# Kernel tuning notes

Measured on AMD Instinct MI355X. Metric: run time of the kernel, lower is better.

Reference implementation:

```python
import jax, jax.numpy as jnp
import numpy as np

NUM_USER = 100000
NUM_ITEM = 50000
N_NODES = NUM_USER + NUM_ITEM
DIM_E = 64
N_EDGES = 2_000_000  # user-item interactions; symmetric adj nnz = 2*N_EDGES
N_LAYERS = 3
DROP_RATE = 0.5
BATCH = 16384


def setup_inputs() -> dict:
    key = jax.random.key(0)
    k_u, k_i, k_ue, k_ie, k_m, k_bu, k_bi = jax.random.split(key, 7)
    # bipartite interaction edges -> symmetric adjacency (COO)
    u = jax.random.randint(k_u, (N_EDGES,), 0, NUM_USER, dtype=jnp.int32)
    it = jax.random.randint(k_i, (N_EDGES,), 0, NUM_ITEM, dtype=jnp.int32) + NUM_USER
    adj_row = jnp.concatenate([u, it])          # [4M]
    adj_col = jnp.concatenate([it, u])          # [4M]
    # symmetric normalization D^-1/2 A D^-1/2
    deg = jnp.zeros((N_NODES,), jnp.float32).at[adj_row].add(1.0) + 1e-7
    dinv = deg ** -0.5
    adj_val = dinv[adj_row] * dinv[adj_col]     # [4M]
    # xavier-uniform-ish embeddings
    ue_scale = (6.0 / (NUM_USER + DIM_E)) ** 0.5
    ie_scale = (6.0 / (NUM_ITEM + DIM_E)) ** 0.5
    user_emb = jax.random.uniform(k_ue, (NUM_USER, DIM_E), jnp.float32, -ue_scale, ue_scale)
    item_emb = jax.random.uniform(k_ie, (NUM_ITEM, DIM_E), jnp.float32, -ie_scale, ie_scale)
    # fixed sparse-dropout keep mask (rate=0.5)
    drop_mask = jax.random.uniform(k_m, (2 * N_EDGES,)) < (1.0 - DROP_RATE)
    users = jax.random.randint(k_bu, (BATCH,), 0, NUM_USER, dtype=jnp.int64)
    items = jax.random.randint(k_bi, (BATCH,), 0, NUM_ITEM, dtype=jnp.int64)
    return {"user_emb": user_emb, "item_emb": item_emb, "adj_val": adj_val,
            "adj_row": adj_row, "adj_col": adj_col, "drop_mask": drop_mask,
            "users": users, "items": items}


def reference(user_emb, item_emb, adj_val, adj_row, adj_col, drop_mask, users, items):
    # sparse dropout: drop entries, rescale kept ones by 1/(1-rate)
    val = jnp.where(drop_mask, adj_val * (1.0 / (1.0 - DROP_RATE)), 0.0)
    ego = jnp.concatenate([user_emb, item_emb], axis=0)   # [N, D]
    acc = ego
    for _ in range(N_LAYERS):
        # SpMM: out[r] += val * ego[c]
        ego = jax.ops.segment_sum(val[:, None] * ego[adj_col], adj_row,
                                  num_segments=N_NODES)
        acc = acc + ego
    all_emb = acc / (N_LAYERS + 1)                        # mean over stacked layers
    user_embeddings = all_emb[users]
    item_embeddings = all_emb[NUM_USER + items]
    return (user_embeddings, item_embeddings)
```

## Files before the change

### kernel.cpp

```cpp
#include <hip/hip_runtime.h>
#include <hip/hip_bf16.h>


#define NUSER 100000
#define NITEM 50000
#define NNODE 150000
#define DIM   64
#define NNZ   4000000
#define BATCH 16384

#define BSH2  9
#define BRWS  512
#define NBK   293
#define SCAP  2048
#define BCAP  16384
#define CHUNK 2048

typedef __hip_bfloat16 bf16;
typedef unsigned short ushort;
typedef unsigned long long u64;
typedef float f4 __attribute__((ext_vector_type(4)));
typedef ushort us4 __attribute__((ext_vector_type(4)));
typedef ushort us8 __attribute__((ext_vector_type(8)));

__device__ __forceinline__ float loadF(const void* p, long i, int isbf16) {
    return isbf16 ? __bfloat162float(((const bf16*)p)[i]) : ((const float*)p)[i];
}

__device__ __forceinline__ bool keepE(const void* mask, int e, int isbyte) {
    return isbyte ? (((const unsigned char*)mask)[e] != 0)
                  : (((const int*)mask)[e] != 0);
}

__device__ __forceinline__ ushort f2bf(float x) {
    unsigned u = __float_as_uint(x);
    return (ushort)((u + 0x7FFFu + ((u >> 16) & 1u)) >> 16);
}
__device__ __forceinline__ float bf2f(ushort u) {
    return __uint_as_float((unsigned)u << 16);
}

__device__ __forceinline__ unsigned encodeV(float v) {
    unsigned fb = __float_as_uint(v);
    unsigned e8 = (fb >> 23) & 0xFFu;
    unsigned m7 = (fb >> 16) & 0x7Fu;
    return ((e8 - 95u) << 7) | m7;
}
__device__ __forceinline__ float decodeV(unsigned code) {
    unsigned vb = code >> 18;
    return __uint_as_float((((vb >> 7) + 95u) << 23) | ((vb & 0x7Fu) << 16));
}

__global__ __launch_bounds__(256) void detect_fmt(const unsigned int* __restrict__ mask,
                                                  const unsigned int* __restrict__ users,
                                                  const unsigned int* __restrict__ adjv,
                                                  int* __restrict__ flags,
                                                  int* __restrict__ bcur) {
    __shared__ int s[3];
    if (threadIdx.x < 3) s[threadIdx.x] = 0;
    for (int b = threadIdx.x; b < 8 * NBK; b += 256) bcur[b] = 0;
    __syncthreads();
    int c0 = 0, c1 = 0, c2 = 0;
    for (int i = threadIdx.x; i < 4096; i += 256) {
        c0 += (mask[i] > 1u) ? 1 : 0;
        if (i & 1) c1 += (users[i] == 0u) ? 1 : 0;
        unsigned lo = adjv[i] & 0xFFFFu;
        unsigned ex = (lo >> 7) & 0xFFu;
        c2 += ((lo >> 15) == 0u && ex >= 0x60u && ex <= 0x7Fu) ? 1 : 0;
    }
    atomicAdd(&s[0], c0); atomicAdd(&s[1], c1); atomicAdd(&s[2], c2);
    __syncthreads();
    if (threadIdx.x == 0) {
        flags[0] = (s[0] > 16) ? 1 : 0;
        flags[1] = (s[1] > 1024) ? 1 : 0;
        flags[2] = (s[2] > 3000) ? 1 : 0;
    }
}

__global__ __launch_bounds__(256) void pass1_partition(const void* __restrict__ mask,
                                                       const int* __restrict__ rows,
                                                       const int* __restrict__ cols,
                                                       const void* __restrict__ adjv,
                                                       const int* __restrict__ flags,
                                                       int* __restrict__ bcur,
                                                       u64* __restrict__ part) {
    __shared__ int cnt[NBK];
    __shared__ int cur[NBK];
    const int isbyte = flags[0];
    const int isbf = flags[2];
    const int base_e = blockIdx.x * CHUNK;
    const int sh = blockIdx.x & 7;
    u64 rec[8];
    int bkt[8];
    unsigned kept = 0;

    for (int b = threadIdx.x; b < NBK; b += 256) cnt[b] = 0;
    __syncthreads();

    #pragma unroll
    for (int k = 0; k < 8; ++k) {
        int e = base_e + k * 256 + threadIdx.x;
        if (e < NNZ && keepE(mask, e, isbyte)) {
            int r = rows[e];
            float v = 2.0f * loadF(adjv, e, isbf);
            rec[k] = (u64)(unsigned)(r & (BRWS - 1))
                   | ((u64)(unsigned)cols[e] << 9)
                   | ((u64)encodeV(v) << 27);
            bkt[k] = r >> BSH2;
            kept |= 1u << k;
            atomicAdd(&cnt[bkt[k]], 1);
        }
    }
    __syncthreads();

    for (int b = threadIdx.x; b < NBK; b += 256)
        cur[b] = cnt[b] ? atomicAdd(&bcur[sh * NBK + b], cnt[b]) : 0;
    __syncthreads();

    #pragma unroll
    for (int k = 0; k < 8; ++k) {
        if (kept & (1u << k)) {
            int pos = atomicAdd(&cur[bkt[k]], 1);
            if (pos < SCAP)
                part[(size_t)bkt[k] * BCAP + sh * SCAP + pos] = rec[k];
        }
    }
}

__global__ __launch_bounds__(512) void bucket_scan(const int* __restrict__ bcur,
                                                   int* __restrict__ gbase,
                                                   int* __restrict__ rowptr) {
    __shared__ int s[512];
    int tid = threadIdx.x;
    int v = 0;
    if (tid < NBK) {
        #pragma unroll
        for (int sh = 0; sh < 8; ++sh) {
            int c = bcur[sh * NBK + tid];
            v += (c > SCAP) ? SCAP : c;
        }
    }
    s[tid] = v;
    __syncthreads();
    for (int off = 1; off < 512; off <<= 1) {
        int t = (tid >= off) ? s[tid - off] : 0;
        __syncthreads();
        s[tid] += t;
        __syncthreads();
    }
    if (tid < NBK) gbase[tid] = s[tid] - v;
    if (tid == 0) rowptr[0] = 0;
}

__global__ __launch_bounds__(512) void pass2_csr(const u64* __restrict__ part,
                                                 const int* __restrict__ bcur,
                                                 const int* __restrict__ gbase,
                                                 unsigned* __restrict__ edges,
                                                 int* __restrict__ rowptr) {
    __shared__ int cnt[BRWS];
    __shared__ int ex[BRWS];
    __shared__ int wsum[512];
    __shared__ int ns[8];
    int b = blockIdx.x;
    int tid = threadIdx.x;
    if (tid < 8) {
        int c = bcur[tid * NBK + b];
        ns[tid] = (c > SCAP) ? SCAP : c;
    }
    const u64* bp = part + (size_t)b * BCAP;
    int gb = gbase[b];

    cnt[tid] = 0;
    __syncthreads();
    #pragma unroll
    for (int sh = 0; sh < 8; ++sh) {
        int n = ns[sh];
        const u64* rp = bp + sh * SCAP;
        for (int j = tid; j < n; j += 512)
            atomicAdd(&cnt[(int)(rp[j] & (BRWS - 1))], 1);
    }
    __syncthreads();

    int c = cnt[tid];
    wsum[tid] = c;
    __syncthreads();
    for (int off = 1; off < 512; off <<= 1) {
        int t = (tid >= off) ? wsum[tid - off] : 0;
        __syncthreads();
        wsum[tid] += t;
        __syncthreads();
    }
    int incl = wsum[tid];
    ex[tid] = incl - c;
    int gr = (b << BSH2) + tid;
    if (gr < NNODE) rowptr[gr + 1] = gb + incl;
    __syncthreads();

    #pragma unroll
    for (int sh = 0; sh < 8; ++sh) {
        int n = ns[sh];
        const u64* rp = bp + sh * SCAP;
        for (int j = tid; j < n; j += 512) {
            u64 rec = rp[j];
            int r = (int)(rec & (BRWS - 1));
            int pos = atomicAdd(&ex[r], 1);
            unsigned col = (unsigned)((rec >> 9) & 0x3FFFFu);
            unsigned code = (unsigned)((rec >> 27) & 0x1FFFu);
            edges[gb + pos] = col | (code << 18);
        }
    }
}

__global__ __launch_bounds__(256) void concat_cast(const void* __restrict__ ue,
                                                   const void* __restrict__ ie,
                                                   const int* __restrict__ flags,
                                                   ushort* __restrict__ A) {
    long q = (long)blockIdx.x * 256 + threadIdx.x;
    const long NU4 = (long)NUSER * DIM / 4;
    const long NT4 = (long)NNODE * DIM / 4;
    if (q >= NT4) return;
    us4 o;
    if (!flags[2]) {
        const f4* s = (q < NU4) ? (const f4*)ue : (const f4*)ie;
        f4 v = s[(q < NU4) ? q : q - NU4];
        o[0] = f2bf(v.x); o[1] = f2bf(v.y); o[2] = f2bf(v.z); o[3] = f2bf(v.w);
    } else {
        const us4* s = (q < NU4) ? (const us4*)ue : (const us4*)ie;
        o = s[(q < NU4) ? q : q - NU4];
    }
    ((us4*)A)[q] = o;
}

__global__ __launch_bounds__(256) void spmm_csr(const ushort* __restrict__ src,
                                                const int* __restrict__ rowptr,
                                                const unsigned* __restrict__ edges,
                                                ushort* __restrict__ dst) {
    int r = blockIdx.x * 32 + (threadIdx.x >> 3);
    if (r >= NNODE) return;
    int t = threadIdx.x & 7;
    int j0 = rowptr[r], j1 = rowptr[r + 1];
    float acc[8] = {0, 0, 0, 0, 0, 0, 0, 0};
    int j = j0;
    for (; j + 4 <= j1; j += 4) {
        unsigned e0 = edges[j];
        unsigned e1 = edges[j + 1];
        unsigned e2 = edges[j + 2];
        unsigned e3 = edges[j + 3];
        us8 s0 = ((const us8*)(src + (size_t)(e0 & 0x3FFFFu) * DIM))[t];
        us8 s1 = ((const us8*)(src + (size_t)(e1 & 0x3FFFFu) * DIM))[t];
        us8 s2 = ((const us8*)(src + (size_t)(e2 & 0x3FFFFu) * DIM))[t];
        us8 s3 = ((const us8*)(src + (size_t)(e3 & 0x3FFFFu) * DIM))[t];
        float v0 = decodeV(e0), v1 = decodeV(e1);
        float v2 = decodeV(e2), v3 = decodeV(e3);
        #pragma unroll
        for (int d = 0; d < 8; ++d) {
            acc[d] += v0 * bf2f(s0[d]);
            acc[d] += v1 * bf2f(s1[d]);
            acc[d] += v2 * bf2f(s2[d]);
            acc[d] += v3 * bf2f(s3[d]);
        }
    }
    for (; j < j1; ++j) {
        unsigned e0 = edges[j];
        float v0 = decodeV(e0);
        us8 s0 = ((const us8*)(src + (size_t)(e0 & 0x3FFFFu) * DIM))[t];
        #pragma unroll
        for (int d = 0; d < 8; ++d) acc[d] += v0 * bf2f(s0[d]);
    }
    us8 o;
    #pragma unroll
    for (int d = 0; d < 8; ++d) o[d] = f2bf(acc[d]);
    __builtin_nontemporal_store(o, (us8*)(dst + (size_t)r * DIM) + t);
}

__device__ __forceinline__ long nodeOf(int b, const int* users, const int* items, int sh) {
    if (b < BATCH) return (long)users[(size_t)b << sh];
    return (long)NUSER + (long)items[(size_t)(b - BATCH) << sh];
}

__global__ __launch_bounds__(256) void gather_first(const ushort* __restrict__ table,
                                                    const int* __restrict__ users,
                                                    const int* __restrict__ items,
                                                    const int* __restrict__ flags,
                                                    float* __restrict__ acc) {
    int t = blockIdx.x * 256 + threadIdx.x;
    if (t >= 2 * BATCH * DIM / 4) return;
    long node = nodeOf(t >> 4, users, items, flags[1]);
    us4 u = ((const us4*)(table + node * DIM))[t & 15];
    f4 a = {bf2f(u[0]), bf2f(u[1]), bf2f(u[2]), bf2f(u[3])};
    ((f4*)acc)[t] = a;
}

__global__ __launch_bounds__(256) void gather_add(const ushort* __restrict__ table,
                                                  const int* __restrict__ users,
                                                  const int* __restrict__ items,
                                                  const int* __restrict__ flags,
                                                  float* __restrict__ acc) {
    int t = blockIdx.x * 256 + threadIdx.x;
    if (t >= 2 * BATCH * DIM / 4) return;
    long node = nodeOf(t >> 4, users, items, flags[1]);
    us4 u = ((const us4*)(table + node * DIM))[t & 15];
    f4 a = ((f4*)acc)[t];
    a.x += bf2f(u[0]); a.y += bf2f(u[1]); a.z += bf2f(u[2]); a.w += bf2f(u[3]);
    ((f4*)acc)[t] = a;
}

__global__ __launch_bounds__(256) void gather_final(const ushort* __restrict__ table,
                                                    const int* __restrict__ users,
                                                    const int* __restrict__ items,
                                                    const int* __restrict__ flags,
                                                    const float* __restrict__ acc,
                                                    float* __restrict__ out) {
    int t = blockIdx.x * 256 + threadIdx.x;
    if (t >= 2 * BATCH * DIM / 4) return;
    long node = nodeOf(t >> 4, users, items, flags[1]);
    us4 u = ((const us4*)(table + node * DIM))[t & 15];
    f4 a = ((const f4*)acc)[t];
    a.x = 0.25f * (a.x + bf2f(u[0]));
    a.y = 0.25f * (a.y + bf2f(u[1]));
    a.z = 0.25f * (a.z + bf2f(u[2]));
    a.w = 0.25f * (a.w + bf2f(u[3]));
    __builtin_nontemporal_store(a, (f4*)out + t);
}

extern "C" void kernel_launch(void* const* d_in, const int* in_sizes, int n_in,
                              void* d_out, int out_size, void* d_ws, size_t ws_size,
                              hipStream_t stream) {
    const void* user_emb = d_in[0];
    const void* item_emb = d_in[1];
    const void* adj_val  = d_in[2];
    const int*  adj_row  = (const int*)d_in[3];
    const int*  adj_col  = (const int*)d_in[4];
    const void* drop_msk = d_in[5];
    const int*  users    = (const int*)d_in[6];
    const int*  items    = (const int*)d_in[7];
    float* out = (float*)d_out;

    char* ws = (char*)d_ws;
    size_t off = 0;
    int* flags = (int*)(ws + off);            off += 256;
    float* out_acc = (float*)(ws + off);      off += (size_t)2 * BATCH * DIM * 4;
    ushort* A = (ushort*)(ws + off);          off += (size_t)NNODE * DIM * 2;
    ushort* B = (ushort*)(ws + off);          off += (size_t)NNODE * DIM * 2;
    int* rowptr = (int*)(ws + off);           off += 600064;
    int* bcur = (int*)(ws + off);             off += 16384;
    int* gbase = (int*)(ws + off);            off += 2048;
    u64* part = (u64*)(ws + off);             off += (size_t)NBK * BCAP * 8;
    unsigned* edges = (unsigned*)(ws + off);  off += (size_t)NNZ * 4;

    const int OUTN4 = 2 * BATCH * DIM / 4;
    const int GOUT = (OUTN4 + 255) / 256;
    const int GP1 = (NNZ + CHUNK - 1) / CHUNK;
    const int GSP = (NNODE + 31) / 32;

    detect_fmt<<<1, 256, 0, stream>>>((const unsigned int*)drop_msk,
                                      (const unsigned int*)users,
                                      (const unsigned int*)adj_val, flags, bcur);
    pass1_partition<<<GP1, 256, 0, stream>>>(drop_msk, adj_row, adj_col, adj_val,
                                             flags, bcur, part);
    bucket_scan<<<1, 512, 0, stream>>>(bcur, gbase, rowptr);
    pass2_csr<<<NBK, 512, 0, stream>>>(part, bcur, gbase, edges, rowptr);
    concat_cast<<<((NNODE * DIM / 4) + 255) / 256, 256, 0, stream>>>(user_emb, item_emb,
                                                                     flags, A);
    gather_first<<<GOUT, 256, 0, stream>>>(A, users, items, flags, out_acc);

    ushort* src = A;
    ushort* dst = B;
    for (int l = 0; l < 3; ++l) {
        spmm_csr<<<GSP, 256, 0, stream>>>(src, rowptr, edges, dst);
        if (l < 2) {
            gather_add<<<GOUT, 256, 0, stream>>>(dst, users, items, flags, out_acc);
        } else {
            gather_final<<<GOUT, 256, 0, stream>>>(dst, users, items, flags, out_acc, out);
        }
        ushort* t = src; src = dst; dst = t;
    }
}
```

Baseline: 202.6 us.

## Fuse partition, cast and first gather into one launch; fold bucket scan into pass2

Merges the edge-partition pass, the embedding concat/cast and the first batch gather into a single kernel with block-range dispatch. The bucket-offset scan moves into every pass2 block, so each block recomputes the prefix sum redundantly. Slot offsets within a block are now taken from the first shared atomic instead of a second round of atomics. The goal is to cut launch count and serialization between small kernels. The cost is redundant scan work in each pass2 block and a gather that reads the original fp32 inputs rather than the cast table.

New measurement: 196.4 us. 3.1% less time.

```diff
diff --git a/kernel.cpp b/kernel.cpp
--- a/kernel.cpp
+++ b/kernel.cpp
@@ -15,6 +15,9 @@
 #define SCAP  2048
 #define BCAP  16384
 #define CHUNK 2048
+#define GP1   1954
+#define GCC   9375
+#define GGF   2048
 
 typedef __hip_bfloat16 bf16;
 typedef unsigned short ushort;
@@ -49,6 +52,11 @@
 __device__ __forceinline__ float decodeV(unsigned code) {
     unsigned vb = code >> 18;
     return __uint_as_float((((vb >> 7) + 95u) << 23) | ((vb & 0x7Fu) << 16));
+}
+
+__device__ __forceinline__ long nodeOf(int b, const int* users, const int* items, int sh) {
+    if (b < BATCH) return (long)users[(size_t)b << sh];
+    return (long)NUSER + (long)items[(size_t)(b - BATCH) << sh];
 }
 
 __global__ __launch_bounds__(256) void detect_fmt(const unsigned int* __restrict__ mask,
@@ -77,101 +85,139 @@
     }
 }
 
-__global__ __launch_bounds__(256) void pass1_partition(const void* __restrict__ mask,
-                                                       const int* __restrict__ rows,
-                                                       const int* __restrict__ cols,
-                                                       const void* __restrict__ adjv,
-                                                       const int* __restrict__ flags,
-                                                       int* __restrict__ bcur,
-                                                       u64* __restrict__ part) {
+__global__ __launch_bounds__(256) void prep_fused(const void* __restrict__ mask,
+                                                  const int* __restrict__ rows,
+                                                  const int* __restrict__ cols,
+                                                  const void* __restrict__ adjv,
+                                                  const void* __restrict__ ue,
+                                                  const void* __restrict__ ie,
+                                                  const int* __restrict__ users,
+                                                  const int* __restrict__ items,
+                                                  const int* __restrict__ flags,
+                                                  int* __restrict__ bcur,
+                                                  u64* __restrict__ part,
+                                                  ushort* __restrict__ A,
+                                                  float* __restrict__ out_acc) {
     __shared__ int cnt[NBK];
     __shared__ int cur[NBK];
-    const int isbyte = flags[0];
-    const int isbf = flags[2];
-    const int base_e = blockIdx.x * CHUNK;
-    const int sh = blockIdx.x & 7;
-    u64 rec[8];
-    int bkt[8];
-    unsigned kept = 0;
-
-    for (int b = threadIdx.x; b < NBK; b += 256) cnt[b] = 0;
-    __syncthreads();
-
-    #pragma unroll
-    for (int k = 0; k < 8; ++k) {
-        int e = base_e + k * 256 + threadIdx.x;
-        if (e < NNZ && keepE(mask, e, isbyte)) {
-            int r = rows[e];
-            float v = 2.0f * loadF(adjv, e, isbf);
-            rec[k] = (u64)(unsigned)(r & (BRWS - 1))
-                   | ((u64)(unsigned)cols[e] << 9)
-                   | ((u64)encodeV(v) << 27);
-            bkt[k] = r >> BSH2;
-            kept |= 1u << k;
-            atomicAdd(&cnt[bkt[k]], 1);
-        }
-    }
-    __syncthreads();
-
-    for (int b = threadIdx.x; b < NBK; b += 256)
-        cur[b] = cnt[b] ? atomicAdd(&bcur[sh * NBK + b], cnt[b]) : 0;
-    __syncthreads();
-
-    #pragma unroll
-    for (int k = 0; k < 8; ++k) {
-        if (kept & (1u << k)) {
-            int pos = atomicAdd(&cur[bkt[k]], 1);
-            if (pos < SCAP)
-                part[(size_t)bkt[k] * BCAP + sh * SCAP + pos] = rec[k];
-        }
-    }
-}
-
-__global__ __launch_bounds__(512) void bucket_scan(const int* __restrict__ bcur,
-                                                   int* __restrict__ gbase,
-                                                   int* __restrict__ rowptr) {
-    __shared__ int s[512];
-    int tid = threadIdx.x;
-    int v = 0;
-    if (tid < NBK) {
-        #pragma unroll
-        for (int sh = 0; sh < 8; ++sh) {
-            int c = bcur[sh * NBK + tid];
-            v += (c > SCAP) ? SCAP : c;
-        }
-    }
-    s[tid] = v;
-    __syncthreads();
-    for (int off = 1; off < 512; off <<= 1) {
-        int t = (tid >= off) ? s[tid - off] : 0;
-        __syncthreads();
-        s[tid] += t;
-        __syncthreads();
-    }
-    if (tid < NBK) gbase[tid] = s[tid] - v;
-    if (tid == 0) rowptr[0] = 0;
+    const int blk = blockIdx.x;
+
+    if (blk < GP1) {
+        const int isbyte = flags[0];
+        const int isbf = flags[2];
+        const int base_e = blk * CHUNK;
+        const int sh = blk & 7;
+        u64 rec[8];
+        int bkt[8], off[8];
+        unsigned kept = 0;
+
+        for (int b = threadIdx.x; b < NBK; b += 256) cnt[b] = 0;
+        __syncthreads();
+
+        #pragma unroll
+        for (int k = 0; k < 8; ++k) {
+            int e = base_e + k * 256 + threadIdx.x;
+            if (e < NNZ && keepE(mask, e, isbyte)) {
+                int r = rows[e];
+                float v = 2.0f * loadF(adjv, e, isbf);
+                rec[k] = (u64)(unsigned)(r & (BRWS - 1))
+                       | ((u64)(unsigned)cols[e] << 9)
+                       | ((u64)encodeV(v) << 27);
+                bkt[k] = r >> BSH2;
+                off[k] = atomicAdd(&cnt[bkt[k]], 1);
+                kept |= 1u << k;
+            }
+        }
+        __syncthreads();
+
+        for (int b = threadIdx.x; b < NBK; b += 256)
+            cur[b] = cnt[b] ? atomicAdd(&bcur[sh * NBK + b], cnt[b]) : 0;
+        __syncthreads();
+
+        #pragma unroll
+        for (int k = 0; k < 8; ++k) {
+            if (kept & (1u << k)) {
+                int pos = cur[bkt[k]] + off[k];
+                if (pos < SCAP)
+                    part[(size_t)bkt[k] * BCAP + sh * SCAP + pos] = rec[k];
+            }
+        }
+    } else if (blk < GP1 + GCC) {
+        long q = (long)(blk - GP1) * 256 + threadIdx.x;
+        const long NU4 = (long)NUSER * DIM / 4;
+        const long NT4 = (long)NNODE * DIM / 4;
+        if (q >= NT4) return;
+        us4 o;
+        if (!flags[2]) {
+            const f4* s = (q < NU4) ? (const f4*)ue : (const f4*)ie;
+            f4 v = s[(q < NU4) ? q : q - NU4];
+            o[0] = f2bf(v.x); o[1] = f2bf(v.y); o[2] = f2bf(v.z); o[3] = f2bf(v.w);
+        } else {
+            const us4* s = (q < NU4) ? (const us4*)ue : (const us4*)ie;
+            o = s[(q < NU4) ? q : q - NU4];
+        }
+        ((us4*)A)[q] = o;
+    } else {
+        int t = (blk - GP1 - GCC) * 256 + threadIdx.x;
+        if (t >= 2 * BATCH * DIM / 4) return;
+        long node = nodeOf(t >> 4, users, items, flags[1]);
+        int d4 = t & 15;
+        const void* src = (node < NUSER) ? ue : ie;
+        long q = (node < NUSER ? node : node - NUSER) * 16 + d4;
+        f4 a;
+        if (!flags[2]) {
+            a = ((const f4*)src)[q];
+        } else {
+            us4 u = ((const us4*)src)[q];
+            a.x = bf2f(u[0]); a.y = bf2f(u[1]); a.z = bf2f(u[2]); a.w = bf2f(u[3]);
+        }
+        ((f4*)out_acc)[t] = a;
+    }
 }
 
 __global__ __launch_bounds__(512) void pass2_csr(const u64* __restrict__ part,
                                                  const int* __restrict__ bcur,
-                                                 const int* __restrict__ gbase,
                                                  unsigned* __restrict__ edges,
                                                  int* __restrict__ rowptr) {
+    __shared__ int tot[512];
     __shared__ int cnt[BRWS];
     __shared__ int ex[BRWS];
     __shared__ int wsum[512];
     __shared__ int ns[8];
+    __shared__ int gb_s, n_s;
     int b = blockIdx.x;
     int tid = threadIdx.x;
+
+    int v = 0;
+    if (tid < NBK) {
+        #pragma unroll
+        for (int sh = 0; sh < 8; ++sh) {
+            int c = bcur[sh * NBK + tid];
+            v += (c > SCAP) ? SCAP : c;
+        }
+    }
+    tot[tid] = v;
     if (tid < 8) {
         int c = bcur[tid * NBK + b];
         ns[tid] = (c > SCAP) ? SCAP : c;
     }
+    cnt[tid] = 0;
+    __syncthreads();
+    for (int off = 1; off < 512; off <<= 1) {
+        int t = (tid >= off) ? tot[tid - off] : 0;
+        __syncthreads();
+        tot[tid] += t;
+        __syncthreads();
+    }
+    if (tid == 0) {
+        gb_s = (b > 0) ? tot[b - 1] : 0;
+        n_s = tot[b] - ((b > 0) ? tot[b - 1] : 0);
+        if (b == 0) rowptr[0] = 0;
+    }
+    __syncthreads();
+    const int gb = gb_s;
     const u64* bp = part + (size_t)b * BCAP;
-    int gb = gbase[b];
-
-    cnt[tid] = 0;
-    __syncthreads();
+
     #pragma unroll
     for (int sh = 0; sh < 8; ++sh) {
         int n = ns[sh];
@@ -209,26 +255,6 @@
             edges[gb + pos] = col | (code << 18);
         }
     }
-}
-
-__global__ __launch_bounds__(256) void concat_cast(const void* __restrict__ ue,
-                                                   const void* __restrict__ ie,
-                                                   const int* __restrict__ flags,
-                                                   ushort* __restrict__ A) {
-    long q = (long)blockIdx.x * 256 + threadIdx.x;
-    const long NU4 = (long)NUSER * DIM / 4;
-    const long NT4 = (long)NNODE * DIM / 4;
-    if (q >= NT4) return;
-    us4 o;
-    if (!flags[2]) {
-        const f4* s = (q < NU4) ? (const f4*)ue : (const f4*)ie;
-        f4 v = s[(q < NU4) ? q : q - NU4];
-        o[0] = f2bf(v.x); o[1] = f2bf(v.y); o[2] = f2bf(v.z); o[3] = f2bf(v.w);
-    } else {
-        const us4* s = (q < NU4) ? (const us4*)ue : (const us4*)ie;
-        o = s[(q < NU4) ? q : q - NU4];
-    }
-    ((us4*)A)[q] = o;
 }
 
 __global__ __launch_bounds__(256) void spmm_csr(const ushort* __restrict__ src,
@@ -273,24 +299,6 @@
     __builtin_nontemporal_store(o, (us8*)(dst + (size_t)r * DIM) + t);
 }
 
-__device__ __forceinline__ long nodeOf(int b, const int* users, const int* items, int sh) {
-    if (b < BATCH) return (long)users[(size_t)b << sh];
-    return (long)NUSER + (long)items[(size_t)(b - BATCH) << sh];
-}
-
-__global__ __launch_bounds__(256) void gather_first(const ushort* __restrict__ table,
-                                                    const int* __restrict__ users,
-                                                    const int* __restrict__ items,
-                                                    const int* __restrict__ flags,
-                                                    float* __restrict__ acc) {
-    int t = blockIdx.x * 256 + threadIdx.x;
-    if (t >= 2 * BATCH * DIM / 4) return;
-    long node = nodeOf(t >> 4, users, items, flags[1]);
-    us4 u = ((const us4*)(table + node * DIM))[t & 15];
-    f4 a = {bf2f(u[0]), bf2f(u[1]), bf2f(u[2]), bf2f(u[3])};
-    ((f4*)acc)[t] = a;
-}
-
 __global__ __launch_bounds__(256) void gather_add(const ushort* __restrict__ table,
                                                   const int* __restrict__ users,
                                                   const int* __restrict__ items,
@@ -344,25 +352,21 @@
     ushort* B = (ushort*)(ws + off);          off += (size_t)NNODE * DIM * 2;
     int* rowptr = (int*)(ws + off);           off += 600064;
     int* bcur = (int*)(ws + off);             off += 16384;
-    int* gbase = (int*)(ws + off);            off += 2048;
     u64* part = (u64*)(ws + off);             off += (size_t)NBK * BCAP * 8;
     unsigned* edges = (unsigned*)(ws + off);  off += (size_t)NNZ * 4;
 
     const int OUTN4 = 2 * BATCH * DIM / 4;
     const int GOUT = (OUTN4 + 255) / 256;
-    const int GP1 = (NNZ + CHUNK - 1) / CHUNK;
     const int GSP = (NNODE + 31) / 32;
 
     detect_fmt<<<1, 256, 0, stream>>>((const unsigned int*)drop_msk,
                                       (const unsigned int*)users,
                                       (const unsigned int*)adj_val, flags, bcur);
-    pass1_partition<<<GP1, 256, 0, stream>>>(drop_msk, adj_row, adj_col, adj_val,
-                                             flags, bcur, part);
-    bucket_scan<<<1, 512, 0, stream>>>(bcur, gbase, rowptr);
-    pass2_csr<<<NBK, 512, 0, stream>>>(part, bcur, gbase, edges, rowptr);
-    concat_cast<<<((NNODE * DIM / 4) + 255) / 256, 256, 0, stream>>>(user_emb, item_emb,
-                                                                     flags, A);
-    gather_first<<<GOUT, 256, 0, stream>>>(A, users, items, flags, out_acc);
+    prep_fused<<<GP1 + GCC + GGF, 256, 0, stream>>>(drop_msk, adj_row, adj_col,
+                                                    adj_val, user_emb, item_emb,
+                                                    users, items, flags, bcur,
+                                                    part, A, out_acc);
+    pass2_csr<<<NBK, 512, 0, stream>>>(part, bcur, edges, rowptr);
 
     ushort* src = A;
     ushort* dst = B;
```
